# Kernel optimization log

Hardware: AMD Instinct MI355X
Metric: run time of the kernel (lower is better)

## Reference

```python
import math
import jax, jax.numpy as jnp
import numpy as np

B, C, T = 8, 512, 4096
DK = max(C // 8, 2)          # 64
SCALE = math.sqrt(DK)        # 8.0
GAMMA = 1.0                  # source inits gamma=0 (identity); use 1.0 to exercise the attention path
EPS = 1e-12


def _l2_normalize(v):
    return v / (jnp.linalg.norm(v) + EPS)


def setup_inputs() -> dict:
    key = jax.random.key(0)
    ks = jax.random.split(key, 5)
    return {
        "x": jax.random.normal(ks[0], (B, C, T), jnp.float32),
        "Wq": jax.random.normal(ks[1], (DK, C), jnp.float32) * 0.05,
        "Wk": jax.random.normal(ks[2], (DK, C), jnp.float32) * 0.05,
        "Wv": jax.random.normal(ks[3], (C, C), jnp.float32) * 0.05,
        "bv": jnp.zeros((C,), jnp.float32),
        "u": jax.random.normal(ks[4], (C,), jnp.float32),
    }


def reference(x, Wq, Wk, Wv, bv, u):
    # spectral norm on value conv weight (one power iteration, u/v as buffers)
    v = jax.lax.stop_gradient(_l2_normalize(Wv.T @ u))
    u2 = jax.lax.stop_gradient(_l2_normalize(Wv @ v))
    sigma = u2 @ (Wv @ v)
    Wv_sn = Wv / sigma

    # 1x1 conv projections
    q = jnp.einsum('dc,bct->btd', Wq, x)               # [B,T,DK]
    k = jnp.einsum('dc,bct->bdt', Wk, x)               # [B,DK,T]
    energy = jnp.einsum('btd,bds->bts', q, k) / SCALE  # [B,T,T]
    attn = jax.nn.softmax(energy, axis=-1)
    val = jnp.einsum('oc,bct->bot', Wv_sn, x) + bv[None, :, None]  # [B,C,T]
    # out = bmm(value, attention^T): out[b,c,t] = sum_s val[b,c,s]*attn[b,t,s]
    out = jnp.einsum('bcs,bts->bct', val, attn)        # [B,C,T]
    return GAMMA * out + x
```

## Files before the change

kernel.cpp:

```cpp
#include <hip/hip_runtime.h>


#define B_  8
#define C_  512
#define T_  4096
#define DK_ 64

typedef __bf16 bf16x8 __attribute__((ext_vector_type(8)));
typedef float  f32x4  __attribute__((ext_vector_type(4)));

static __device__ __forceinline__ unsigned short f2bf(float f) {
  unsigned u = __float_as_uint(f);
  u += 0x7fffu + ((u >> 16) & 1u);
  return (unsigned short)(u >> 16);
}

static __device__ __forceinline__ unsigned cvt_pk_bf16(float a, float b) {
  unsigned r;
  asm("v_cvt_pk_bf16_f32 %0, %1, %2" : "=v"(r) : "v"(a), "v"(b));
  return r;
}

#define BAR_LDS() asm volatile("s_waitcnt lgkmcnt(0)\ns_barrier" ::: "memory")

__global__ void sigma_kernel(const float* __restrict__ Wv,
                             const float* __restrict__ u,
                             float* __restrict__ sig) {
  __shared__ float red[512];
  __shared__ float vsh[512];
  __shared__ float snorm;
  int tid = threadIdx.x;

  vsh[tid] = u[tid];
  __syncthreads();
  float acc = 0.f;
  for (int j = 0; j < 512; ++j) acc += Wv[(size_t)j * 512 + tid] * vsh[j];
  red[tid] = acc * acc;
  __syncthreads();
  for (int s = 256; s >= 1; s >>= 1) {
    if (tid < s) red[tid] += red[tid + s];
    __syncthreads();
  }
  if (tid == 0) snorm = sqrtf(red[0]) + 1e-12f;
  __syncthreads();
  float v = acc / snorm;
  __syncthreads();
  vsh[tid] = v;
  __syncthreads();
  float wacc = 0.f;
  for (int c = 0; c < 512; ++c) wacc += Wv[(size_t)tid * 512 + c] * vsh[c];
  red[tid] = wacc * wacc;
  __syncthreads();
  for (int s = 256; s >= 1; s >>= 1) {
    if (tid < s) red[tid] += red[tid + s];
    __syncthreads();
  }
  if (tid == 0) {
    float ww = red[0];
    float sigma = ww / (sqrtf(ww) + 1e-12f);
    sig[0] = 1.f / sigma;
  }
}

__global__ __launch_bounds__(128)
void castw_kernel(const float* __restrict__ Wq, const float* __restrict__ Wk,
                  const float* __restrict__ Wv, const float* __restrict__ sig,
                  unsigned short* __restrict__ Wc) {
  int row = blockIdx.x;
  int c = threadIdx.x * 4;
  const float* src;
  float s;
  if (row < 64) {
    src = Wq + (size_t)row * 512;
    s = 1.4426950408889634f / 8.0f;
  } else if (row < 128) {
    src = Wk + (size_t)(row - 64) * 512;
    s = 1.0f;
  } else {
    src = Wv + (size_t)(row - 128) * 512;
    s = sig[0];
  }
  float4 v = *reinterpret_cast<const float4*>(src + c);
  ushort4 o;
  o.x = f2bf(v.x * s);
  o.y = f2bf(v.y * s);
  o.z = f2bf(v.z * s);
  o.w = f2bf(v.w * s);
  *reinterpret_cast<ushort4*>(Wc + (size_t)row * 512 + c) = o;
}

__global__ __launch_bounds__(256)
void castt_kernel(const float* __restrict__ x, unsigned short* __restrict__ xT) {
  __shared__ __align__(16) unsigned short ldsT[64][72];
  int tid = threadIdx.x;
  int t0 = blockIdx.x * 64, c0 = blockIdx.y * 64, b = blockIdx.z;
  const float* xb = x + ((size_t)b * C_ + c0) * T_ + t0;
#pragma unroll
  for (int k2 = 0; k2 < 4; ++k2) {
    int idx = k2 * 256 + tid;
    int c = idx >> 4, t4 = (idx & 15) * 4;
    float4 v = *reinterpret_cast<const float4*>(xb + (size_t)c * T_ + t4);
    ldsT[t4 + 0][c] = f2bf(v.x);
    ldsT[t4 + 1][c] = f2bf(v.y);
    ldsT[t4 + 2][c] = f2bf(v.z);
    ldsT[t4 + 3][c] = f2bf(v.w);
  }
  __syncthreads();
  unsigned short* xTb = xT + ((size_t)b * T_ + t0) * C_ + c0;
#pragma unroll
  for (int k2 = 0; k2 < 2; ++k2) {
    int idx = k2 * 256 + tid;
    int t = idx >> 3, ch = idx & 7;
    bf16x8 v = *reinterpret_cast<const bf16x8*>(&ldsT[t][ch * 8]);
    *reinterpret_cast<bf16x8*>(xTb + (size_t)t * C_ + ch * 8) = v;
  }
}

__global__ __launch_bounds__(512, 2)
void proj_kernel(const unsigned short* __restrict__ Wc,
                 const unsigned short* __restrict__ xT,
                 const float* __restrict__ bv,
                 unsigned short* __restrict__ Q,
                 unsigned short* __restrict__ Kk,
                 unsigned short* __restrict__ V) {
  __shared__ __align__(16) char smem[98304];
  const int tid = threadIdx.x;
  const int w = tid >> 6;
  const int lane = tid & 63;
  const int col = lane & 15;
  const int g = lane >> 4;
  const int b = blockIdx.x & 7;
  const int t0 = (blockIdx.x >> 3) * 128;

  const unsigned short* xTb = xT + ((size_t)b * T_ + t0) * C_;

  auto stageX = [&](int bsel, int kc) {
    int off = w * 1024 + lane * 16;
    int tl = off >> 6;
    int cb = off & 63;
    const unsigned short* src = xTb + (size_t)tl * C_ + kc + cb / 2;
    __builtin_amdgcn_global_load_lds(
        (const __attribute__((address_space(1))) unsigned int*)src,
        (__attribute__((address_space(3))) unsigned int*)(smem + bsel * 8192 + off),
        16, 0, 0);
  };
  auto stageW = [&](int bsel, int kc) {
#pragma unroll
    for (int i = 0; i < 5; ++i) {
      int off = i * 8192 + w * 1024 + lane * 16;
      int o = off >> 6;
      int cb = off & 63;
      const unsigned short* src = Wc + (size_t)o * 512 + kc + cb / 2;
      __builtin_amdgcn_global_load_lds(
          (const __attribute__((address_space(1))) unsigned int*)src,
          (__attribute__((address_space(3))) unsigned int*)(smem + 16384 + bsel * 40960 + off),
          16, 0, 0);
    }
  };

  f32x4 acc[5][8];
#pragma unroll
  for (int of = 0; of < 5; ++of)
#pragma unroll
    for (int j = 0; j < 8; ++j) acc[of][j] = (f32x4){0.f, 0.f, 0.f, 0.f};

  stageX(0, 0);
  stageW(0, 0);
  __syncthreads();
  int cur = 0;

  for (int ks = 0; ks < 16; ++ks) {
    int kc = ks * 32;
    if (ks < 15) {
      stageX(cur ^ 1, kc + 32);
      stageW(cur ^ 1, kc + 32);
    }
    bf16x8 af[5], bfr[8];
#pragma unroll
    for (int of = 0; of < 5; ++of) {
      int o = w * 80 + of * 16 + col;
      af[of] = *reinterpret_cast<const bf16x8*>(smem + 16384 + cur * 40960 + o * 64 + g * 16);
    }
#pragma unroll
    for (int j = 0; j < 8; ++j) {
      int tl = 16 * j + col;
      bfr[j] = *reinterpret_cast<const bf16x8*>(smem + cur * 8192 + tl * 64 + g * 16);
    }
#pragma unroll
    for (int of = 0; of < 5; ++of)
#pragma unroll
      for (int j = 0; j < 8; ++j)
        acc[of][j] = __builtin_amdgcn_mfma_f32_16x16x32_bf16(af[of], bfr[j], acc[of][j], 0, 0, 0);
    __syncthreads();
    cur ^= 1;
  }

  unsigned short* qkt = (unsigned short*)smem;
  unsigned short* vt = (unsigned short*)(smem + 34816 + w * 4352);
  unsigned short* Vb = V + (size_t)b * C_ * T_;

#pragma unroll
  for (int of = 0; of < 5; ++of) {
    int o0 = w * 80 + of * 16;
    if (o0 < 128) {
#pragma unroll
      for (int j = 0; j < 8; ++j)
#pragma unroll
        for (int r = 0; r < 4; ++r)
          qkt[(16 * j + col) * 136 + o0 + g * 4 + r] = f2bf(acc[of][j][r]);
    } else {
      int c0 = o0 - 128;
      float bvr[4];
#pragma unroll
      for (int r = 0; r < 4; ++r) bvr[r] = bv[c0 + g * 4 + r];
#pragma unroll
      for (int j = 0; j < 8; ++j)
#pragma unroll
        for (int r = 0; r < 4; ++r)
          vt[(g * 4 + r) * 136 + 16 * j + col] = f2bf(acc[of][j][r] + bvr[r]);
#pragma unroll
      for (int p = 0; p < 4; ++p) {
        int o_r = p * 4 + g;
        bf16x8 v8 = *reinterpret_cast<const bf16x8*>((char*)vt + o_r * 272 + col * 16);
        *reinterpret_cast<bf16x8*>(Vb + (size_t)(c0 + o_r) * T_ + t0 + col * 8) = v8;
      }
    }
  }
  __syncthreads();
  unsigned short* Qb = Q + (size_t)b * T_ * DK_;
  unsigned short* Kb = Kk + (size_t)b * T_ * DK_;
#pragma unroll
  for (int k2 = 0; k2 < 2; ++k2) {
    int idx = k2 * 512 + tid;
    int t = idx >> 3, ch = idx & 7;
    bf16x8 q8 = *reinterpret_cast<const bf16x8*>(&qkt[t * 136 + ch * 8]);
    *reinterpret_cast<bf16x8*>(Qb + (size_t)(t0 + t) * DK_ + ch * 8) = q8;
    bf16x8 k8 = *reinterpret_cast<const bf16x8*>(&qkt[t * 136 + 64 + ch * 8]);
    *reinterpret_cast<bf16x8*>(Kb + (size_t)(t0 + t) * DK_ + ch * 8) = k8;
  }
}

__global__ __launch_bounds__(512, 2)
void flash_kernel(const unsigned short* __restrict__ Q,
                  const unsigned short* __restrict__ Kk,
                  const unsigned short* __restrict__ V,
                  const float* __restrict__ x, float* __restrict__ out) {
  __shared__ __align__(16) unsigned short p_lds[2][128 * 64];
  __shared__ __align__(16) float scale_lds[2][8][16];
  __shared__ __align__(16) float l_lds[128];
  __shared__ unsigned long long flags_lds[2];

  const int tid = threadIdx.x;
  const int w = tid >> 6;
  const int lane = tid & 63;
  const int col = lane & 15;
  const int g = lane >> 4;
  const int b = blockIdx.x & 7;
  const int t0 = (blockIdx.x >> 3) * 128;
  const int trow0 = t0 + w * 16;

  const unsigned short* Qb = Q + (size_t)b * T_ * DK_;
  const unsigned short* Kb = Kk + (size_t)b * T_ * DK_;
  const unsigned short* Vb = V + (size_t)b * C_ * T_;

  bf16x8 qf[2];
  {
    const unsigned short* qrow = Qb + (size_t)(trow0 + col) * DK_ + g * 8;
    qf[0] = *reinterpret_cast<const bf16x8*>(qrow);
    qf[1] = *reinterpret_cast<const bf16x8*>(qrow + 32);
  }

  bf16x8 kf[2][4];
  auto loadK = [&](int s0) {
#pragma unroll
    for (int ks = 0; ks < 2; ++ks)
#pragma unroll
      for (int j = 0; j < 4; ++j)
        kf[ks][j] = *reinterpret_cast<const bf16x8*>(
            Kb + (size_t)(s0 + col + 16 * j) * DK_ + 32 * ks + g * 8);
  };
  bf16x8 vf[2][4];
  auto loadV = [&](int s0) {
#pragma unroll
    for (int ks = 0; ks < 2; ++ks)
#pragma unroll
      for (int ct = 0; ct < 4; ++ct)
        vf[ks][ct] = *reinterpret_cast<const bf16x8*>(
            Vb + (size_t)(64 * w + 16 * ct + col) * T_ + s0 + 32 * ks + 8 * g);
  };

  float m_run = -1e30f, l_run = 0.f;
  f32x4 o_acc[8][4];
#pragma unroll
  for (int qt = 0; qt < 8; ++qt)
#pragma unroll
    for (int ct = 0; ct < 4; ++ct) o_acc[qt][ct] = (f32x4){0.f, 0.f, 0.f, 0.f};

  loadK(0);
  loadV(0);

  const float RTHR = 10.0f;
  const int prow = w * 16 + col;
  const int pswz = (prow & 7) << 4;

  for (int it = 0; it < T_ / 64; ++it) {
    const int par = it & 1;
    char* pbase = (char*)p_lds + par * 16384;

    f32x4 sacc[4];
#pragma unroll
    for (int j = 0; j < 4; ++j) sacc[j] = (f32x4){0.f, 0.f, 0.f, 0.f};
#pragma unroll
    for (int ks = 0; ks < 2; ++ks)
#pragma unroll
      for (int j = 0; j < 4; ++j)
        sacc[j] = __builtin_amdgcn_mfma_f32_16x16x32_bf16(kf[ks][j], qf[ks], sacc[j], 0, 0, 0);

    if (it + 1 < T_ / 64) loadK(64 * (it + 1));

    float v0 = fmaxf(fmaxf(sacc[0][0], sacc[0][1]), sacc[0][2]);
    float v1 = fmaxf(fmaxf(sacc[0][3], sacc[1][0]), sacc[1][1]);
    float v2 = fmaxf(fmaxf(sacc[1][2], sacc[1][3]), sacc[2][0]);
    float v3 = fmaxf(fmaxf(sacc[2][1], sacc[2][2]), sacc[2][3]);
    float v4 = fmaxf(fmaxf(sacc[3][0], sacc[3][1]), sacc[3][2]);
    float tm = fmaxf(fmaxf(fmaxf(v0, v1), fmaxf(v2, v3)), fmaxf(v4, sacc[3][3]));
    tm = fmaxf(tm, __shfl_xor(tm, 16));
    tm = fmaxf(tm, __shfl_xor(tm, 32));

    int wave_any = __any(tm > m_run + RTHR);
    float sc = 1.0f;
    if (wave_any) {
      float m_new = fmaxf(m_run, tm);
      sc = __builtin_amdgcn_exp2f(m_run - m_new);
      m_run = m_new;
      if (lane < 16) scale_lds[par][w][lane] = sc;
    }
    if (lane == 0)
      ((volatile unsigned char*)&flags_lds[par])[w] = (unsigned char)wave_any;

    float rs = 0.f;
    char* prow_base = pbase + prow * 128;
#pragma unroll
    for (int j = 0; j < 4; ++j) {
      float p0 = __builtin_amdgcn_exp2f(sacc[j][0] - m_run);
      float p1 = __builtin_amdgcn_exp2f(sacc[j][1] - m_run);
      float p2 = __builtin_amdgcn_exp2f(sacc[j][2] - m_run);
      float p3 = __builtin_amdgcn_exp2f(sacc[j][3] - m_run);
      rs += (p0 + p1) + (p2 + p3);
      uint2 pk2 = {cvt_pk_bf16(p0, p1), cvt_pk_bf16(p2, p3)};
      *reinterpret_cast<uint2*>(prow_base + (((16 * j + 4 * g) * 2) ^ pswz)) = pk2;
    }
    rs += __shfl_xor(rs, 16);
    rs += __shfl_xor(rs, 32);
    l_run = l_run * sc + rs;

    BAR_LDS();

    unsigned long long fl = flags_lds[par];
    if (fl) {
#pragma unroll
      for (int qt = 0; qt < 8; ++qt)
        if ((fl >> (8 * qt)) & 0xffull) {
          f32x4 s4 = *reinterpret_cast<const f32x4*>(&scale_lds[par][qt][4 * g]);
#pragma unroll
          for (int ct = 0; ct < 4; ++ct) o_acc[qt][ct] *= s4;
        }
    }

    __builtin_amdgcn_s_setprio(1);
#pragma unroll
    for (int ks = 0; ks < 2; ++ks) {
#pragma unroll
      for (int qt = 0; qt < 8; ++qt) {
        int row = 16 * qt + col;
        bf16x8 pa = *reinterpret_cast<const bf16x8*>(
            pbase + row * 128 + ((64 * ks + 16 * g) ^ ((row & 7) << 4)));
#pragma unroll
        for (int ct = 0; ct < 4; ++ct)
          o_acc[qt][ct] = __builtin_amdgcn_mfma_f32_16x16x32_bf16(pa, vf[ks][ct], o_acc[qt][ct], 0, 0, 0);
      }
    }
    __builtin_amdgcn_s_setprio(0);

    if (it + 1 < T_ / 64) loadV(64 * (it + 1));
  }

  if (lane < 16) l_lds[w * 16 + lane] = l_run;
  BAR_LDS();

  const float* xb = x + (size_t)b * C_ * T_;
  float* ob = out + (size_t)b * C_ * T_;
#pragma unroll
  for (int qt = 0; qt < 8; ++qt) {
    f32x4 l4 = *reinterpret_cast<const f32x4*>(&l_lds[16 * qt + 4 * g]);
    f32x4 linv;
#pragma unroll
    for (int r = 0; r < 4; ++r) linv[r] = 1.f / l4[r];
#pragma unroll
    for (int ct = 0; ct < 4; ++ct) {
      size_t idx = (size_t)(64 * w + 16 * ct + col) * T_ + t0 + 16 * qt + 4 * g;
      f32x4 xv = *reinterpret_cast<const f32x4*>(xb + idx);
      f32x4 o = o_acc[qt][ct];
#pragma unroll
      for (int r = 0; r < 4; ++r) o[r] = o[r] * linv[r] + xv[r];
      *reinterpret_cast<f32x4*>(ob + idx) = o;
    }
  }
}

extern "C" void kernel_launch(void* const* d_in, const int* in_sizes, int n_in,
                              void* d_out, int out_size, void* d_ws, size_t ws_size,
                              hipStream_t stream) {
  const float* x  = (const float*)d_in[0];
  const float* Wq = (const float*)d_in[1];
  const float* Wk = (const float*)d_in[2];
  const float* Wv = (const float*)d_in[3];
  const float* bv = (const float*)d_in[4];
  const float* u  = (const float*)d_in[5];
  float* out = (float*)d_out;

  char* ws = (char*)d_ws;
  float* sig = (float*)ws;
  unsigned short* Q  = (unsigned short*)(ws + 1024);
  unsigned short* Kk = (unsigned short*)(ws + 1024 + (size_t)4 * 1024 * 1024);
  unsigned short* V  = (unsigned short*)(ws + 1024 + (size_t)8 * 1024 * 1024);
  unsigned short* xT = (unsigned short*)(ws + 1024 + (size_t)40 * 1024 * 1024);
  unsigned short* Wc = (unsigned short*)(ws + 1024 + (size_t)72 * 1024 * 1024);

  sigma_kernel<<<1, 512, 0, stream>>>(Wv, u, sig);
  castw_kernel<<<640, 128, 0, stream>>>(Wq, Wk, Wv, sig, Wc);
  castt_kernel<<<dim3(T_ / 64, C_ / 64, B_), 256, 0, stream>>>(x, xT);
  proj_kernel<<<256, 512, 0, stream>>>(Wc, xT, bv, Q, Kk, V);
  flash_kernel<<<256, 512, 0, stream>>>(Q, Kk, V, x, out);
}
```

Measured before the change: 414.1 us.

## Split flash kernel over channel halves with LDS-staged K and asm V loads

Each flash block now handles 64 query rows and one 256-channel half, using 256 threads and launching 1024 blocks instead of 256 blocks of 128 rows by 512 channels. K tiles are double-buffered into LDS with global_load_lds, and V fragments come from inline-asm global loads that use a scalar base plus per-lane offsets. The aim is more parallelism, lower register pressure from the smaller accumulator, and K/V fetches overlapped with softmax work. In exchange, QK^T and softmax are computed twice per query row, once per channel half, and a vmcnt(0) wait before each barrier may stall on the V loads.

```diff
diff --git a/kernel.cpp b/kernel.cpp
--- a/kernel.cpp
+++ b/kernel.cpp
@@ -21,7 +21,16 @@
   return r;
 }
 
+static __device__ __forceinline__ unsigned long long rfl64(const void* p) {
+  unsigned long long a = (unsigned long long)p;
+  unsigned lo = __builtin_amdgcn_readfirstlane((unsigned)a);
+  unsigned hi = __builtin_amdgcn_readfirstlane((unsigned)(a >> 32));
+  return ((unsigned long long)hi << 32) | lo;
+}
+
 #define BAR_LDS() asm volatile("s_waitcnt lgkmcnt(0)\ns_barrier" ::: "memory")
+#define WAIT_VM0() do { asm volatile("s_waitcnt vmcnt(0)" ::: "memory"); \
+                        __builtin_amdgcn_sched_barrier(0); } while (0)
 
 __global__ void sigma_kernel(const float* __restrict__ Wv,
                              const float* __restrict__ u,
@@ -240,64 +249,86 @@
   }
 }
 
-__global__ __launch_bounds__(512, 2)
+__global__ __launch_bounds__(256, 2)
 void flash_kernel(const unsigned short* __restrict__ Q,
                   const unsigned short* __restrict__ Kk,
                   const unsigned short* __restrict__ V,
                   const float* __restrict__ x, float* __restrict__ out) {
-  __shared__ __align__(16) unsigned short p_lds[2][128 * 64];
-  __shared__ __align__(16) float scale_lds[2][8][16];
-  __shared__ __align__(16) float l_lds[128];
-  __shared__ unsigned long long flags_lds[2];
+  __shared__ __align__(16) unsigned short k_lds[2][64 * 64];
+  __shared__ __align__(16) unsigned short p_lds[2][64 * 64];
+  __shared__ __align__(16) float scale_lds[2][4][16];
+  __shared__ __align__(16) float l_lds[64];
+  __shared__ unsigned flags_lds[2];
 
   const int tid = threadIdx.x;
   const int w = tid >> 6;
   const int lane = tid & 63;
   const int col = lane & 15;
   const int g = lane >> 4;
-  const int b = blockIdx.x & 7;
-  const int t0 = (blockIdx.x >> 3) * 128;
+  const int bid = blockIdx.x;
+  const int b = bid & 7;
+  const int cs = (bid >> 3) & 1;
+  const int t0 = (bid >> 4) * 64;
   const int trow0 = t0 + w * 16;
 
   const unsigned short* Qb = Q + (size_t)b * T_ * DK_;
   const unsigned short* Kb = Kk + (size_t)b * T_ * DK_;
   const unsigned short* Vb = V + (size_t)b * C_ * T_;
 
-  bf16x8 qf[2];
+  auto stageK = [&](int par, int s0) {
+#pragma unroll
+    for (int n = 0; n < 2; ++n) {
+      int o = n * 4096 + tid * 16;
+      int s = o >> 7;
+      int z = (o & 127) ^ ((s & 7) << 4);
+      const char* src = (const char*)Kb + (size_t)(s0 + s) * 128 + z;
+      __builtin_amdgcn_global_load_lds(
+          (const __attribute__((address_space(1))) unsigned int*)src,
+          (__attribute__((address_space(3))) unsigned int*)((char*)k_lds[par] + o),
+          16, 0, 0);
+    }
+  };
+
+  bf16x8 qf0, qf1;
   {
     const unsigned short* qrow = Qb + (size_t)(trow0 + col) * DK_ + g * 8;
-    qf[0] = *reinterpret_cast<const bf16x8*>(qrow);
-    qf[1] = *reinterpret_cast<const bf16x8*>(qrow + 32);
-  }
-
-  bf16x8 kf[2][4];
-  auto loadK = [&](int s0) {
-#pragma unroll
-    for (int ks = 0; ks < 2; ++ks)
-#pragma unroll
-      for (int j = 0; j < 4; ++j)
-        kf[ks][j] = *reinterpret_cast<const bf16x8*>(
-            Kb + (size_t)(s0 + col + 16 * j) * DK_ + 32 * ks + g * 8);
-  };
-  bf16x8 vf[2][4];
-  auto loadV = [&](int s0) {
-#pragma unroll
-    for (int ks = 0; ks < 2; ++ks)
-#pragma unroll
-      for (int ct = 0; ct < 4; ++ct)
-        vf[ks][ct] = *reinterpret_cast<const bf16x8*>(
-            Vb + (size_t)(64 * w + 16 * ct + col) * T_ + s0 + 32 * ks + 8 * g);
-  };
+    qf0 = *reinterpret_cast<const bf16x8*>(qrow);
+    qf1 = *reinterpret_cast<const bf16x8*>(qrow + 32);
+    asm volatile("" : "+v"(qf0), "+v"(qf1));
+  }
+
+  const unsigned long long vbase = rfl64(Vb + (size_t)(cs * 256 + w * 64) * T_);
+  unsigned vo0 = (16 * 0 + col) * 8192 + 16 * g;
+  unsigned vo1 = (16 * 1 + col) * 8192 + 16 * g;
+  unsigned vo2 = (16 * 2 + col) * 8192 + 16 * g;
+  unsigned vo3 = (16 * 3 + col) * 8192 + 16 * g;
+
+  bf16x8 vf00, vf10, vf01, vf11, vf02, vf12, vf03, vf13;
+
+#define ISSUE_V()                                                          \
+  asm volatile(                                                            \
+      "global_load_dwordx4 %0, %8, %12\n\t"                                \
+      "global_load_dwordx4 %1, %8, %12 offset:64\n\t"                      \
+      "global_load_dwordx4 %2, %9, %12\n\t"                                \
+      "global_load_dwordx4 %3, %9, %12 offset:64\n\t"                      \
+      "global_load_dwordx4 %4, %10, %12\n\t"                               \
+      "global_load_dwordx4 %5, %10, %12 offset:64\n\t"                     \
+      "global_load_dwordx4 %6, %11, %12\n\t"                               \
+      "global_load_dwordx4 %7, %11, %12 offset:64\n\t"                     \
+      : "=&v"(vf00), "=&v"(vf10), "=&v"(vf01), "=&v"(vf11),                \
+        "=&v"(vf02), "=&v"(vf12), "=&v"(vf03), "=&v"(vf13)                 \
+      : "v"(vo0), "v"(vo1), "v"(vo2), "v"(vo3), "s"(vbase))
 
   float m_run = -1e30f, l_run = 0.f;
-  f32x4 o_acc[8][4];
-#pragma unroll
-  for (int qt = 0; qt < 8; ++qt)
+  f32x4 o_acc[4][4];
+#pragma unroll
+  for (int qt = 0; qt < 4; ++qt)
 #pragma unroll
     for (int ct = 0; ct < 4; ++ct) o_acc[qt][ct] = (f32x4){0.f, 0.f, 0.f, 0.f};
 
-  loadK(0);
-  loadV(0);
+  stageK(0, 0);
+  asm volatile("s_waitcnt vmcnt(0)" ::: "memory");
+  __syncthreads();
 
   const float RTHR = 10.0f;
   const int prow = w * 16 + col;
@@ -305,25 +336,36 @@
 
   for (int it = 0; it < T_ / 64; ++it) {
     const int par = it & 1;
-    char* pbase = (char*)p_lds + par * 16384;
+    char* pbase = (char*)p_lds + par * 8192;
+    const char* kbl = (const char*)k_lds + par * 8192;
+
+    bf16x8 kf[2][4];
+#pragma unroll
+    for (int ks = 0; ks < 2; ++ks)
+#pragma unroll
+      for (int j = 0; j < 4; ++j)
+        kf[ks][j] = *reinterpret_cast<const bf16x8*>(
+            kbl + (col + 16 * j) * 128 + ((64 * ks + 16 * g) ^ ((col & 7) << 4)));
 
     f32x4 sacc[4];
 #pragma unroll
     for (int j = 0; j < 4; ++j) sacc[j] = (f32x4){0.f, 0.f, 0.f, 0.f};
 #pragma unroll
-    for (int ks = 0; ks < 2; ++ks)
-#pragma unroll
-      for (int j = 0; j < 4; ++j)
-        sacc[j] = __builtin_amdgcn_mfma_f32_16x16x32_bf16(kf[ks][j], qf[ks], sacc[j], 0, 0, 0);
-
-    if (it + 1 < T_ / 64) loadK(64 * (it + 1));
-
-    float v0 = fmaxf(fmaxf(sacc[0][0], sacc[0][1]), sacc[0][2]);
-    float v1 = fmaxf(fmaxf(sacc[0][3], sacc[1][0]), sacc[1][1]);
-    float v2 = fmaxf(fmaxf(sacc[1][2], sacc[1][3]), sacc[2][0]);
-    float v3 = fmaxf(fmaxf(sacc[2][1], sacc[2][2]), sacc[2][3]);
-    float v4 = fmaxf(fmaxf(sacc[3][0], sacc[3][1]), sacc[3][2]);
-    float tm = fmaxf(fmaxf(fmaxf(v0, v1), fmaxf(v2, v3)), fmaxf(v4, sacc[3][3]));
+    for (int j = 0; j < 4; ++j)
+      sacc[j] = __builtin_amdgcn_mfma_f32_16x16x32_bf16(kf[0][j], qf0, sacc[j], 0, 0, 0);
+#pragma unroll
+    for (int j = 0; j < 4; ++j)
+      sacc[j] = __builtin_amdgcn_mfma_f32_16x16x32_bf16(kf[1][j], qf1, sacc[j], 0, 0, 0);
+
+    stageK(par ^ 1, 64 * (it + 1));
+    ISSUE_V();
+
+    float u0 = fmaxf(fmaxf(sacc[0][0], sacc[0][1]), sacc[0][2]);
+    float u1 = fmaxf(fmaxf(sacc[0][3], sacc[1][0]), sacc[1][1]);
+    float u2 = fmaxf(fmaxf(sacc[1][2], sacc[1][3]), sacc[2][0]);
+    float u3 = fmaxf(fmaxf(sacc[2][1], sacc[2][2]), sacc[2][3]);
+    float u4 = fmaxf(fmaxf(sacc[3][0], sacc[3][1]), sacc[3][2]);
+    float tm = fmaxf(fmaxf(fmaxf(u0, u1), fmaxf(u2, u3)), fmaxf(u4, sacc[3][3]));
     tm = fmaxf(tm, __shfl_xor(tm, 16));
     tm = fmaxf(tm, __shfl_xor(tm, 32));
 
@@ -354,13 +396,14 @@
     rs += __shfl_xor(rs, 32);
     l_run = l_run * sc + rs;
 
+    WAIT_VM0();
     BAR_LDS();
 
-    unsigned long long fl = flags_lds[par];
+    unsigned fl = flags_lds[par];
     if (fl) {
 #pragma unroll
-      for (int qt = 0; qt < 8; ++qt)
-        if ((fl >> (8 * qt)) & 0xffull) {
+      for (int qt = 0; qt < 4; ++qt)
+        if ((fl >> (8 * qt)) & 0xffu) {
           f32x4 s4 = *reinterpret_cast<const f32x4*>(&scale_lds[par][qt][4 * g]);
 #pragma unroll
           for (int ct = 0; ct < 4; ++ct) o_acc[qt][ct] *= s4;
@@ -369,36 +412,43 @@
 
     __builtin_amdgcn_s_setprio(1);
 #pragma unroll
-    for (int ks = 0; ks < 2; ++ks) {
-#pragma unroll
-      for (int qt = 0; qt < 8; ++qt) {
-        int row = 16 * qt + col;
-        bf16x8 pa = *reinterpret_cast<const bf16x8*>(
-            pbase + row * 128 + ((64 * ks + 16 * g) ^ ((row & 7) << 4)));
-#pragma unroll
-        for (int ct = 0; ct < 4; ++ct)
-          o_acc[qt][ct] = __builtin_amdgcn_mfma_f32_16x16x32_bf16(pa, vf[ks][ct], o_acc[qt][ct], 0, 0, 0);
-      }
+    for (int qt = 0; qt < 4; ++qt) {
+      int row = 16 * qt + col;
+      const char* pr = pbase + row * 128;
+      int swz = (row & 7) << 4;
+      bf16x8 pa0 = *reinterpret_cast<const bf16x8*>(pr + ((16 * g) ^ swz));
+      bf16x8 pa1 = *reinterpret_cast<const bf16x8*>(pr + ((64 + 16 * g) ^ swz));
+      o_acc[qt][0] = __builtin_amdgcn_mfma_f32_16x16x32_bf16(pa0, vf00, o_acc[qt][0], 0, 0, 0);
+      o_acc[qt][1] = __builtin_amdgcn_mfma_f32_16x16x32_bf16(pa0, vf01, o_acc[qt][1], 0, 0, 0);
+      o_acc[qt][2] = __builtin_amdgcn_mfma_f32_16x16x32_bf16(pa0, vf02, o_acc[qt][2], 0, 0, 0);
+      o_acc[qt][3] = __builtin_amdgcn_mfma_f32_16x16x32_bf16(pa0, vf03, o_acc[qt][3], 0, 0, 0);
+      o_acc[qt][0] = __builtin_amdgcn_mfma_f32_16x16x32_bf16(pa1, vf10, o_acc[qt][0], 0, 0, 0);
+      o_acc[qt][1] = __builtin_amdgcn_mfma_f32_16x16x32_bf16(pa1, vf11, o_acc[qt][1], 0, 0, 0);
+      o_acc[qt][2] = __builtin_amdgcn_mfma_f32_16x16x32_bf16(pa1, vf12, o_acc[qt][2], 0, 0, 0);
+      o_acc[qt][3] = __builtin_amdgcn_mfma_f32_16x16x32_bf16(pa1, vf13, o_acc[qt][3], 0, 0, 0);
     }
     __builtin_amdgcn_s_setprio(0);
 
-    if (it + 1 < T_ / 64) loadV(64 * (it + 1));
-  }
+    vo0 += 128; vo1 += 128; vo2 += 128; vo3 += 128;
+  }
+
+  asm volatile("s_waitcnt vmcnt(0)" ::: "memory");
 
   if (lane < 16) l_lds[w * 16 + lane] = l_run;
   BAR_LDS();
 
   const float* xb = x + (size_t)b * C_ * T_;
   float* ob = out + (size_t)b * C_ * T_;
-#pragma unroll
-  for (int qt = 0; qt < 8; ++qt) {
+  const int cb = cs * 256 + w * 64;
+#pragma unroll
+  for (int qt = 0; qt < 4; ++qt) {
     f32x4 l4 = *reinterpret_cast<const f32x4*>(&l_lds[16 * qt + 4 * g]);
     f32x4 linv;
 #pragma unroll
     for (int r = 0; r < 4; ++r) linv[r] = 1.f / l4[r];
 #pragma unroll
     for (int ct = 0; ct < 4; ++ct) {
-      size_t idx = (size_t)(64 * w + 16 * ct + col) * T_ + t0 + 16 * qt + 4 * g;
+      size_t idx = (size_t)(cb + 16 * ct + col) * T_ + t0 + 16 * qt + 4 * g;
       f32x4 xv = *reinterpret_cast<const f32x4*>(xb + idx);
       f32x4 o = o_acc[qt][ct];
 #pragma unroll
@@ -406,6 +456,7 @@
       *reinterpret_cast<f32x4*>(ob + idx) = o;
     }
   }
+#undef ISSUE_V
 }
 
 extern "C" void kernel_launch(void* const* d_in, const int* in_sizes, int n_in,
@@ -431,5 +482,5 @@
   castw_kernel<<<640, 128, 0, stream>>>(Wq, Wk, Wv, sig, Wc);
   castt_kernel<<<dim3(T_ / 64, C_ / 64, B_), 256, 0, stream>>>(x, xT);
   proj_kernel<<<256, 512, 0, stream>>>(Wc, xT, bv, Q, Kk, V);
-  flash_kernel<<<256, 512, 0, stream>>>(Q, Kk, V, x, out);
-}
+  flash_kernel<<<1024, 256, 0, stream>>>(Q, Kk, V, x, out);
+}
```

Measured after the change: 396.4 us. 1.04x faster.
